# Performance work log

Hardware: AMD Instinct MI355X
Metric: run time of the kernel (lower is better)

## Reference

```python
import jax, jax.numpy as jnp
import numpy as np


def setup_inputs() -> dict:
    key = jax.random.key(0)
    k1, k2 = jax.random.split(key)
    b, c, h, w = 16, 2048, 32, 32
    n_points = 64
    fea = jax.random.normal(k1, (b, c, h, w), dtype=jnp.float32)
    point_list = jax.random.uniform(k2, (n_points, 2), dtype=jnp.float32)  # (x, y) in [0,1)
    valid = jnp.ones((n_points,), dtype=bool)
    return {"fea": fea, "point_list": point_list, "valid": valid}


def reference(fea, point_list, valid):
    # forward_point of SimModel, with fea == backbone(x)['feat4']
    b, c, h, w = fea.shape
    # point_cur = [int(px*w), int(py*h)]  (points in [0,1) so trunc == floor)
    ix = jnp.clip((point_list[:, 0] * w).astype(jnp.int32), 0, w - 1)  # [P]
    iy = jnp.clip((point_list[:, 1] * h).astype(jnp.int32), 0, h - 1)  # [P]
    # gather query feature vectors at each point: [b, c, P]
    queries = fea[:, :, iy, ix]
    # cosine-normalize keys (over channel) and queries
    keys = fea / jnp.linalg.norm(fea, axis=1, keepdims=True)          # [b, c, h, w]
    q = queries / jnp.linalg.norm(queries, axis=1, keepdims=True)    # [b, c, P]
    # cosine-similarity attention over all h*w locations: [b, P, h*w]
    attn = jnp.einsum('bcp,bck->bpk', q, keys.reshape(b, c, h * w))
    # torch: attn = (attn - attn.min(-1)[0]) / attn.max(-1)[0]
    # (RHS fully evaluated first -> both min and max taken on the ORIGINAL attn)
    amin = attn.min(axis=-1, keepdims=True)
    amax = attn.max(axis=-1, keepdims=True)
    attn = (attn - amin) / amax
    soft_masks = attn.reshape(b, -1, h, w)                            # [b, P, h, w]
    # invalid points produce all-zero masks
    return jnp.where(valid[None, :, None, None], soft_masks, jnp.zeros((), soft_masks.dtype))
```

## Files before the change

### kernel.cpp

```cpp
#include <hip/hip_runtime.h>

#define BB 16
#define CC 2048
#define HH 32
#define WW 32
#define HW 1024
#define NP 64

#define PCH 32
#define NCH (CC/PCH)

#define KB 64
#define CT 64
#define BP 68

typedef __bf16 bf16x8  __attribute__((ext_vector_type(8)));
typedef float  f32x4   __attribute__((ext_vector_type(4)));
typedef float  f32x16  __attribute__((ext_vector_type(16)));

__device__ __forceinline__ unsigned f2bf2(float lo, float hi) {
    unsigned a = __float_as_uint(lo);
    unsigned b = __float_as_uint(hi);
    a += 0x7fffu + ((a >> 16) & 1u);
    b += 0x7fffu + ((b >> 16) & 1u);
    return (a >> 16) | (b & 0xffff0000u);
}


__global__ __launch_bounds__(256) void prep_kernel(const float* __restrict__ fea,
                                                   const float* __restrict__ pl,
                                                   unsigned short* __restrict__ qbf,
                                                   float* __restrict__ np2) {
    int cch = blockIdx.x, b = blockIdx.y;
    int t = threadIdx.x, lane = t & 63, rr = t >> 6;

    int ix = (int)(pl[2 * lane + 0] * WW); ix = min(max(ix, 0), WW - 1);
    int iy = (int)(pl[2 * lane + 1] * HH); iy = min(max(iy, 0), HH - 1);
    int kp = iy * WW + ix;

    __shared__ unsigned short buf[2][4][HW];
    __shared__ unsigned short ex[NP][PCH + 4];

    float ssq[16];
#pragma unroll
    for (int i = 0; i < 16; ++i) ssq[i] = 0.f;

    const float* base = fea + ((size_t)b * CC + cch * PCH + rr) * HW + 4 * lane;

#pragma unroll
    for (int ph = 0; ph < PCH / 4; ++ph) {
        float4 fv[4];
#pragma unroll
        for (int s = 0; s < 4; ++s)
            fv[s] = *(const float4*)(base + (size_t)(ph * 4) * HW + 256 * s);
#pragma unroll
        for (int s = 0; s < 4; ++s) {
            ssq[4 * s + 0] += fv[s].x * fv[s].x;
            ssq[4 * s + 1] += fv[s].y * fv[s].y;
            ssq[4 * s + 2] += fv[s].z * fv[s].z;
            ssq[4 * s + 3] += fv[s].w * fv[s].w;
            uint2 pk;
            pk.x = f2bf2(fv[s].x, fv[s].y);
            pk.y = f2bf2(fv[s].z, fv[s].w);
            *(uint2*)&buf[ph & 1][rr][4 * lane + 256 * s] = pk;
        }
        __syncthreads();
        ex[lane][ph * 4 + rr] = buf[ph & 1][rr][kp];
    }
    __syncthreads();

    float* red = (float*)buf;
#pragma unroll
    for (int s = 0; s < 4; ++s) {
        f32x4 v = {ssq[4 * s + 0], ssq[4 * s + 1], ssq[4 * s + 2], ssq[4 * s + 3]};
        *(f32x4*)&red[rr * HW + 4 * lane + 256 * s] = v;
    }
    __syncthreads();
    {
        int k0 = 4 * t;
        f32x4 r0 = *(f32x4*)&red[0 * HW + k0];
        f32x4 r1 = *(f32x4*)&red[1 * HW + k0];
        f32x4 r2 = *(f32x4*)&red[2 * HW + k0];
        f32x4 r3 = *(f32x4*)&red[3 * HW + k0];
        f32x4 sum = (r0 + r1) + (r2 + r3);
        *(f32x4*)&np2[((size_t)cch * BB + b) * HW + k0] = sum;
    }
    {
        int p = t >> 2, part = t & 3;
        uint2 lo = *(uint2*)&ex[p][8 * part];
        uint2 hi = *(uint2*)&ex[p][8 * part + 4];
        uint4 o = make_uint4(lo.x, lo.y, hi.x, hi.y);
        *(uint4*)&qbf[((size_t)b * NP + p) * CC + cch * PCH + 8 * part] = o;
    }
}

__global__ __launch_bounds__(128) void nred_kernel(const float* __restrict__ np2,
                                                   float* __restrict__ rn) {
    int b = blockIdx.y;
    int k = blockIdx.x * 128 + threadIdx.x;
    float s = 0.f;
#pragma unroll 8
    for (int cch = 0; cch < NCH; ++cch)
        s += np2[((size_t)cch * BB + b) * HW + k];
    rn[(size_t)b * HW + k] = rsqrtf(s);
}

template<int NCS>
__global__ __launch_bounds__(256) void gemm_kernel(const float* __restrict__ fea,
                                                   const unsigned short* __restrict__ qbf,
                                                   float* __restrict__ dotp) {
    constexpr int CHALF = CC / NCS;
    constexpr int NST = CHALF / CT;
    constexpr int CSB = (NCS == 4) ? 2 : 1;

    int id = blockIdx.x + (int)gridDim.x * blockIdx.y;
    int cpx = (16 * NCS * BB) >> 3;
    int sid = (id & 7) * cpx + (id >> 3);
    int kc = sid & 15;
    int cs = (sid >> 4) & (NCS - 1);
    int b  = sid >> (4 + CSB);

    int t = threadIdx.x, lane = t & 63, w = t >> 6;
    int pt = w >> 1, kt = w & 1;
    int p0 = 32 * pt;
    int k0 = KB * kc;
    int c0 = cs * CHALF;
    int lo = lane & 31, hi = lane >> 5;

    __shared__ __align__(16) unsigned short bt[2][CT][BP];

    int sc = t >> 2, sq = t & 3;
    const float* gsrc = fea + ((size_t)b * CC + c0 + sc) * HW + k0 + 16 * sq;

    const unsigned short* qb = qbf + ((size_t)b * NP + p0 + lo) * CC + c0 + 8 * hi;

    f32x16 acc = {};
    union UA { int4 i; bf16x8 v; };

    float4 g[4];
#pragma unroll
    for (int h = 0; h < 4; ++h) g[h] = *(const float4*)(gsrc + 4 * h);
    UA a_cur[4], a_nxt[4];
#pragma unroll
    for (int cw = 0; cw < 4; ++cw) a_cur[cw].i = *(const int4*)(qb + 16 * cw);

    for (int s = 0; s < NST; ++s) {
        int cur = s & 1;
#pragma unroll
        for (int h = 0; h < 4; ++h) {
            uint2 pk;
            pk.x = f2bf2(g[h].x, g[h].y);
            pk.y = f2bf2(g[h].z, g[h].w);
            *(uint2*)&bt[cur][sc][16 * sq + 4 * h] = pk;
        }
        __syncthreads();

        int sn = (s + 1 < NST) ? s + 1 : s;
#pragma unroll
        for (int h = 0; h < 4; ++h)
            g[h] = *(const float4*)(gsrc + (size_t)sn * CT * HW + 4 * h);
#pragma unroll
        for (int cw = 0; cw < 4; ++cw)
            a_nxt[cw].i = *(const int4*)(qb + (size_t)sn * CT + 16 * cw);

#pragma unroll
        for (int cw = 0; cw < 4; ++cw) {
            union { unsigned short u[8]; bf16x8 v; } bf;
#pragma unroll
            for (int e = 0; e < 8; ++e)
                bf.u[e] = bt[cur][16 * cw + 8 * hi + e][32 * kt + lo];
            acc = __builtin_amdgcn_mfma_f32_32x32x16_bf16(a_cur[cw].v, bf.v, acc, 0, 0, 0);
        }
#pragma unroll
        for (int cw = 0; cw < 4; ++cw) a_cur[cw] = a_nxt[cw];
    }

    float* dbase = dotp + (((size_t)cs * BB + b) * NP) * HW;
#pragma unroll
    for (int r = 0; r < 16; ++r) {
        int p = p0 + (r & 3) + 8 * (r >> 2) + 4 * hi;
        dbase[(size_t)p * HW + k0 + 32 * kt + lo] = acc[r];
    }
}

template<int NCS>
__global__ __launch_bounds__(256) void finalize_kernel(const float* __restrict__ dotp,
                                                       const float* __restrict__ rn,
                                                       const float* __restrict__ pl,
                                                       const int* __restrict__ valid,
                                                       float* __restrict__ out) {
    int p = blockIdx.x, b = blockIdx.y;
    int t = threadIdx.x;
    int k0 = 4 * t;

    int ix = (int)(pl[2 * p + 0] * WW); ix = min(max(ix, 0), WW - 1);
    int iy = (int)(pl[2 * p + 1] * HH); iy = min(max(iy, 0), HH - 1);
    int kp = iy * WW + ix;
    float rnp = rn[(size_t)b * HW + kp];

    f32x4 d = {0.f, 0.f, 0.f, 0.f};
#pragma unroll
    for (int cs = 0; cs < NCS; ++cs)
        d += *(const f32x4*)(dotp + (((size_t)cs * BB + b) * NP + p) * HW + k0);
    float4 rk = *(const float4*)&rn[(size_t)b * HW + k0];

    float val[4];
    val[0] = d[0] * rk.x * rnp;
    val[1] = d[1] * rk.y * rnp;
    val[2] = d[2] * rk.z * rnp;
    val[3] = d[3] * rk.w * rnp;

    float mn = fminf(fminf(val[0], val[1]), fminf(val[2], val[3]));
    float mx = fmaxf(fmaxf(val[0], val[1]), fmaxf(val[2], val[3]));
#pragma unroll
    for (int off = 32; off; off >>= 1) {
        mn = fminf(mn, __shfl_xor(mn, off));
        mx = fmaxf(mx, __shfl_xor(mx, off));
    }
    __shared__ float smn[4], smx[4];
    int wave = t >> 6;
    if ((t & 63) == 0) { smn[wave] = mn; smx[wave] = mx; }
    __syncthreads();
    mn = fminf(fminf(smn[0], smn[1]), fminf(smn[2], smn[3]));
    mx = fmaxf(fmaxf(smx[0], smx[1]), fmaxf(smx[2], smx[3]));

    bool vld = valid[p] != 0;
    float4 o;
    o.x = vld ? (val[0] - mn) / mx : 0.f;
    o.y = vld ? (val[1] - mn) / mx : 0.f;
    o.z = vld ? (val[2] - mn) / mx : 0.f;
    o.w = vld ? (val[3] - mn) / mx : 0.f;
    *(float4*)&out[((size_t)b * NP + p) * HW + k0] = o;
}

extern "C" void kernel_launch(void* const* d_in, const int* in_sizes, int n_in,
                              void* d_out, int out_size, void* d_ws, size_t ws_size,
                              hipStream_t stream) {
    const float* fea = (const float*)d_in[0];
    const float* pl  = (const float*)d_in[1];
    const int* valid = (const int*)d_in[2];
    float* out = (float*)d_out;

    unsigned short* qbf = (unsigned short*)d_ws;
    float* np2 = (float*)(qbf + (size_t)BB * NP * CC);
    float* rn  = np2 + (size_t)NCH * BB * HW;
    float* dotp = rn + (size_t)BB * HW;

    const size_t base_b = ((size_t)BB * NP * CC) * 2 + ((size_t)NCH * BB * HW + (size_t)BB * HW) * 4;
    const size_t need4 = base_b + (size_t)4 * BB * NP * HW * 4;

    prep_kernel<<<dim3(NCH, BB), 256, 0, stream>>>(fea, pl, qbf, np2);
    nred_kernel<<<dim3(8, BB), 128, 0, stream>>>(np2, rn);
    if (ws_size >= need4) {
        gemm_kernel<4><<<dim3(64, BB), 256, 0, stream>>>(fea, qbf, dotp);
        finalize_kernel<4><<<dim3(NP, BB), 256, 0, stream>>>(dotp, rn, pl, valid, out);
    } else {
        gemm_kernel<2><<<dim3(32, BB), 256, 0, stream>>>(fea, qbf, dotp);
        finalize_kernel<2><<<dim3(NP, BB), 256, 0, stream>>>(dotp, rn, pl, valid, out);
    }
}
```

Measured before the change: 64.23 us.

## Pre-pack features to channel-interleaved bf16 and feed MFMA directly from global

Adds a prep pass that converts the feature map once into a bf16 layout with 8 channels interleaved per spatial location, plus per-chunk squared norms. A separate gather kernel builds the query vectors. The GEMM then loads MFMA B operands straight from this packed buffer, with no LDS staging, barriers or per-tile fp32-to-bf16 conversion. This needs a larger workspace plus an extra 64MB write and read, and it falls back to the old path when the workspace is too small.

```diff
diff --git a/kernel.cpp b/kernel.cpp
--- a/kernel.cpp
+++ b/kernel.cpp
@@ -7,9 +7,7 @@
 #define HW 1024
 #define NP 64
 
-#define PCH 32
-#define NCH (CC/PCH)
-
+#define NCH 64
 #define KB 64
 #define CT 64
 #define BP 68
@@ -27,6 +25,119 @@
 }
 
 
+__global__ __launch_bounds__(256) void prepT_kernel(const float* __restrict__ fea,
+                                                    unsigned short* __restrict__ feaP,
+                                                    float* __restrict__ np2) {
+    int cch = blockIdx.x, b = blockIdx.y;
+    int t = threadIdx.x;
+    int c0 = cch * 32;
+
+    const float* fb = fea + ((size_t)b * CC + c0) * HW + t;
+    unsigned short* fp = feaP + (((size_t)b * 256 + (c0 >> 3)) * HW + t) * 8;
+
+    float ssq[4] = {0.f, 0.f, 0.f, 0.f};
+
+#pragma unroll
+    for (int c8 = 0; c8 < 4; ++c8) {
+#pragma unroll
+        for (int m = 0; m < 4; ++m) {
+            float v[8];
+#pragma unroll
+            for (int e = 0; e < 8; ++e)
+                v[e] = fb[(size_t)(8 * c8 + e) * HW + 256 * m];
+            float s = 0.f;
+#pragma unroll
+            for (int e = 0; e < 8; ++e) s += v[e] * v[e];
+            ssq[m] += s;
+            uint4 o;
+            o.x = f2bf2(v[0], v[1]); o.y = f2bf2(v[2], v[3]);
+            o.z = f2bf2(v[4], v[5]); o.w = f2bf2(v[6], v[7]);
+            *(uint4*)&fp[((size_t)c8 * HW + 256 * m) * 8] = o;
+        }
+    }
+#pragma unroll
+    for (int m = 0; m < 4; ++m)
+        np2[((size_t)cch * BB + b) * HW + t + 256 * m] = ssq[m];
+}
+
+__global__ __launch_bounds__(256) void qgather_kernel(const unsigned short* __restrict__ feaP,
+                                                      const float* __restrict__ pl,
+                                                      unsigned short* __restrict__ qbf) {
+    int p = blockIdx.x, b = blockIdx.y, t = threadIdx.x;
+    int ix = (int)(pl[2 * p + 0] * WW); ix = min(max(ix, 0), WW - 1);
+    int iy = (int)(pl[2 * p + 1] * HH); iy = min(max(iy, 0), HH - 1);
+    int kp = iy * WW + ix;
+    uint4 v = *(const uint4*)&feaP[(((size_t)b * 256 + t) * HW + kp) * 8];
+    *(uint4*)&qbf[((size_t)(b * NP + p)) * CC + 8 * t] = v;
+}
+
+__global__ __launch_bounds__(128) void nred_kernel(const float* __restrict__ np2,
+                                                   float* __restrict__ rn) {
+    int b = blockIdx.y;
+    int k = blockIdx.x * 128 + threadIdx.x;
+    float s = 0.f;
+#pragma unroll 8
+    for (int cch = 0; cch < NCH; ++cch)
+        s += np2[((size_t)cch * BB + b) * HW + k];
+    rn[(size_t)b * HW + k] = rsqrtf(s);
+}
+
+template<int NCS>
+__global__ __launch_bounds__(256) void gemmf_kernel(const unsigned short* __restrict__ feaP,
+                                                    const unsigned short* __restrict__ qbf,
+                                                    float* __restrict__ dotp) {
+    constexpr int CHALF = CC / NCS;
+    constexpr int NST = CHALF / CT;
+    constexpr int CSB = (NCS == 4) ? 2 : 1;
+
+    int id = blockIdx.x + (int)gridDim.x * blockIdx.y;
+    int cpx = (16 * NCS * BB) >> 3;
+    int sid = (id & 7) * cpx + (id >> 3);
+    int kc = sid & 15;
+    int cs = (sid >> 4) & (NCS - 1);
+    int b  = sid >> (4 + CSB);
+
+    int t = threadIdx.x, lane = t & 63, w = t >> 6;
+    int pt = w >> 1, kt = w & 1;
+    int p0 = 32 * pt, k0 = KB * kc, c0 = cs * CHALF;
+    int lo = lane & 31, hi = lane >> 5;
+
+    const unsigned short* qb = qbf + ((size_t)(b * NP + p0 + lo)) * CC + c0 + 8 * hi;
+    const unsigned short* fp = feaP + (((size_t)b * 256 + (c0 >> 3) + hi) * HW
+                                       + k0 + 32 * kt + lo) * 8;
+
+    f32x16 acc = {};
+    union U { int4 i; bf16x8 v; };
+    U a_cur[4], b_cur[4], a_nxt[4], b_nxt[4];
+
+#pragma unroll
+    for (int cw = 0; cw < 4; ++cw) {
+        a_cur[cw].i = *(const int4*)(qb + 16 * cw);
+        b_cur[cw].i = *(const int4*)(fp + (size_t)(2 * cw) * (HW * 8));
+    }
+
+    for (int s = 0; s < NST; ++s) {
+        int sn = (s + 1 < NST) ? s + 1 : s;
+#pragma unroll
+        for (int cw = 0; cw < 4; ++cw) {
+            a_nxt[cw].i = *(const int4*)(qb + sn * CT + 16 * cw);
+            b_nxt[cw].i = *(const int4*)(fp + (size_t)(8 * sn + 2 * cw) * (HW * 8));
+        }
+#pragma unroll
+        for (int cw = 0; cw < 4; ++cw)
+            acc = __builtin_amdgcn_mfma_f32_32x32x16_bf16(a_cur[cw].v, b_cur[cw].v, acc, 0, 0, 0);
+#pragma unroll
+        for (int cw = 0; cw < 4; ++cw) { a_cur[cw] = a_nxt[cw]; b_cur[cw] = b_nxt[cw]; }
+    }
+
+    float* dbase = dotp + (((size_t)cs * BB + b) * NP) * HW;
+#pragma unroll
+    for (int r = 0; r < 16; ++r) {
+        int p = p0 + (r & 3) + 8 * (r >> 2) + 4 * hi;
+        dbase[(size_t)p * HW + k0 + 32 * kt + lo] = acc[r];
+    }
+}
+
 __global__ __launch_bounds__(256) void prep_kernel(const float* __restrict__ fea,
                                                    const float* __restrict__ pl,
                                                    unsigned short* __restrict__ qbf,
@@ -39,16 +150,16 @@
     int kp = iy * WW + ix;
 
     __shared__ unsigned short buf[2][4][HW];
-    __shared__ unsigned short ex[NP][PCH + 4];
+    __shared__ unsigned short ex[NP][32 + 4];
 
     float ssq[16];
 #pragma unroll
     for (int i = 0; i < 16; ++i) ssq[i] = 0.f;
 
-    const float* base = fea + ((size_t)b * CC + cch * PCH + rr) * HW + 4 * lane;
-
-#pragma unroll
-    for (int ph = 0; ph < PCH / 4; ++ph) {
+    const float* base = fea + ((size_t)b * CC + cch * 32 + rr) * HW + 4 * lane;
+
+#pragma unroll
+    for (int ph = 0; ph < 8; ++ph) {
         float4 fv[4];
 #pragma unroll
         for (int s = 0; s < 4; ++s)
@@ -90,49 +201,29 @@
         uint2 lo = *(uint2*)&ex[p][8 * part];
         uint2 hi = *(uint2*)&ex[p][8 * part + 4];
         uint4 o = make_uint4(lo.x, lo.y, hi.x, hi.y);
-        *(uint4*)&qbf[((size_t)b * NP + p) * CC + cch * PCH + 8 * part] = o;
-    }
-}
-
-__global__ __launch_bounds__(128) void nred_kernel(const float* __restrict__ np2,
-                                                   float* __restrict__ rn) {
-    int b = blockIdx.y;
-    int k = blockIdx.x * 128 + threadIdx.x;
-    float s = 0.f;
-#pragma unroll 8
-    for (int cch = 0; cch < NCH; ++cch)
-        s += np2[((size_t)cch * BB + b) * HW + k];
-    rn[(size_t)b * HW + k] = rsqrtf(s);
-}
-
-template<int NCS>
-__global__ __launch_bounds__(256) void gemm_kernel(const float* __restrict__ fea,
-                                                   const unsigned short* __restrict__ qbf,
-                                                   float* __restrict__ dotp) {
-    constexpr int CHALF = CC / NCS;
-    constexpr int NST = CHALF / CT;
-    constexpr int CSB = (NCS == 4) ? 2 : 1;
-
+        *(uint4*)&qbf[((size_t)(b * NP + p)) * CC + cch * 32 + 8 * part] = o;
+    }
+}
+
+__global__ __launch_bounds__(256) void gemm_lds_kernel(const float* __restrict__ fea,
+                                                       const unsigned short* __restrict__ qbf,
+                                                       float* __restrict__ dotp) {
+    constexpr int NCS = 2, CHALF = CC / 2, NST = CHALF / CT;
     int id = blockIdx.x + (int)gridDim.x * blockIdx.y;
     int cpx = (16 * NCS * BB) >> 3;
     int sid = (id & 7) * cpx + (id >> 3);
-    int kc = sid & 15;
-    int cs = (sid >> 4) & (NCS - 1);
-    int b  = sid >> (4 + CSB);
+    int kc = sid & 15, cs = (sid >> 4) & 1, b = sid >> 5;
 
     int t = threadIdx.x, lane = t & 63, w = t >> 6;
     int pt = w >> 1, kt = w & 1;
-    int p0 = 32 * pt;
-    int k0 = KB * kc;
-    int c0 = cs * CHALF;
+    int p0 = 32 * pt, k0 = KB * kc, c0 = cs * CHALF;
     int lo = lane & 31, hi = lane >> 5;
 
     __shared__ __align__(16) unsigned short bt[2][CT][BP];
 
     int sc = t >> 2, sq = t & 3;
     const float* gsrc = fea + ((size_t)b * CC + c0 + sc) * HW + k0 + 16 * sq;
-
-    const unsigned short* qb = qbf + ((size_t)b * NP + p0 + lo) * CC + c0 + 8 * hi;
+    const unsigned short* qb = qbf + ((size_t)(b * NP + p0 + lo)) * CC + c0 + 8 * hi;
 
     f32x16 acc = {};
     union UA { int4 i; bf16x8 v; };
@@ -154,7 +245,6 @@
             *(uint2*)&bt[cur][sc][16 * sq + 4 * h] = pk;
         }
         __syncthreads();
-
         int sn = (s + 1 < NST) ? s + 1 : s;
 #pragma unroll
         for (int h = 0; h < 4; ++h)
@@ -162,7 +252,6 @@
 #pragma unroll
         for (int cw = 0; cw < 4; ++cw)
             a_nxt[cw].i = *(const int4*)(qb + (size_t)sn * CT + 16 * cw);
-
 #pragma unroll
         for (int cw = 0; cw < 4; ++cw) {
             union { unsigned short u[8]; bf16x8 v; } bf;
@@ -230,7 +319,7 @@
     o.y = vld ? (val[1] - mn) / mx : 0.f;
     o.z = vld ? (val[2] - mn) / mx : 0.f;
     o.w = vld ? (val[3] - mn) / mx : 0.f;
-    *(float4*)&out[((size_t)b * NP + p) * HW + k0] = o;
+    *(float4*)&out[((size_t)(b * NP + p)) * HW + k0] = o;
 }
 
 extern "C" void kernel_launch(void* const* d_in, const int* in_sizes, int n_in,
@@ -245,17 +334,23 @@
     float* np2 = (float*)(qbf + (size_t)BB * NP * CC);
     float* rn  = np2 + (size_t)NCH * BB * HW;
     float* dotp = rn + (size_t)BB * HW;
-
-    const size_t base_b = ((size_t)BB * NP * CC) * 2 + ((size_t)NCH * BB * HW + (size_t)BB * HW) * 4;
-    const size_t need4 = base_b + (size_t)4 * BB * NP * HW * 4;
-
-    prep_kernel<<<dim3(NCH, BB), 256, 0, stream>>>(fea, pl, qbf, np2);
-    nred_kernel<<<dim3(8, BB), 128, 0, stream>>>(np2, rn);
-    if (ws_size >= need4) {
-        gemm_kernel<4><<<dim3(64, BB), 256, 0, stream>>>(fea, qbf, dotp);
+    unsigned short* feaP = (unsigned short*)(dotp + (size_t)4 * BB * NP * HW);
+
+    const size_t needP = (size_t)BB * NP * CC * 2
+                       + ((size_t)NCH * BB * HW + (size_t)BB * HW) * 4
+                       + (size_t)4 * BB * NP * HW * 4
+                       + (size_t)BB * (CC / 8) * HW * 8 * 2;
+
+    if (ws_size >= needP) {
+        prepT_kernel<<<dim3(NCH, BB), 256, 0, stream>>>(fea, feaP, np2);
+        qgather_kernel<<<dim3(NP, BB), 256, 0, stream>>>(feaP, pl, qbf);
+        nred_kernel<<<dim3(8, BB), 128, 0, stream>>>(np2, rn);
+        gemmf_kernel<4><<<dim3(64, BB), 256, 0, stream>>>(feaP, qbf, dotp);
         finalize_kernel<4><<<dim3(NP, BB), 256, 0, stream>>>(dotp, rn, pl, valid, out);
     } else {
-        gemm_kernel<2><<<dim3(32, BB), 256, 0, stream>>>(fea, qbf, dotp);
+        prep_kernel<<<dim3(NCH, BB), 256, 0, stream>>>(fea, pl, qbf, np2);
+        nred_kernel<<<dim3(8, BB), 128, 0, stream>>>(np2, rn);
+        gemm_lds_kernel<<<dim3(32, BB), 256, 0, stream>>>(fea, qbf, dotp);
         finalize_kernel<2><<<dim3(NP, BB), 256, 0, stream>>>(dotp, rn, pl, valid, out);
     }
 }
```

Measured after the change: 72.22 us. 1.12x slower.

## Stage bf16 copy of features in prep kernel and feed GEMM from it

Applied to the files above, without the earlier changes.

The prep kernel, which already converts features to bf16 for the query extraction, now also writes a full bf16 copy of the feature map to workspace. A new GEMM kernel loads these bf16 tiles directly into LDS instead of re-reading fp32 features and converting them. The aim is to halve the bytes the GEMM reads and drop its conversion ALU work, at the cost of an extra 64MB write in prep. The channel split is also fixed at 2 instead of 4, which halves the partial-product traffic into the finalize kernel but also halves the GEMM grid size. The fallback path launches the same GEMM twice.

```diff
diff --git a/kernel.cpp b/kernel.cpp
--- a/kernel.cpp
+++ b/kernel.cpp
@@ -9,9 +9,11 @@
 
 #define PCH 32
 #define NCH (CC/PCH)
-
 #define KB 64
 #define CT 64
+#define NCS 2
+#define CHALF (CC/NCS)
+#define NST (CHALF/CT)
 #define BP 68
 
 typedef __bf16 bf16x8  __attribute__((ext_vector_type(8)));
@@ -27,10 +29,12 @@
 }
 
 
+template<bool WRITE_FB16>
 __global__ __launch_bounds__(256) void prep_kernel(const float* __restrict__ fea,
                                                    const float* __restrict__ pl,
                                                    unsigned short* __restrict__ qbf,
-                                                   float* __restrict__ np2) {
+                                                   float* __restrict__ np2,
+                                                   unsigned short* __restrict__ fb16) {
     int cch = blockIdx.x, b = blockIdx.y;
     int t = threadIdx.x, lane = t & 63, rr = t >> 6;
 
@@ -63,6 +67,10 @@
             pk.x = f2bf2(fv[s].x, fv[s].y);
             pk.y = f2bf2(fv[s].z, fv[s].w);
             *(uint2*)&buf[ph & 1][rr][4 * lane + 256 * s] = pk;
+            if (WRITE_FB16) {
+                *(uint2*)&fb16[((size_t)b * CC + cch * PCH + ph * 4 + rr) * HW
+                               + 4 * lane + 256 * s] = pk;
+            }
         }
         __syncthreads();
         ex[lane][ph * 4 + rr] = buf[ph & 1][rr][kp];
@@ -90,7 +98,7 @@
         uint2 lo = *(uint2*)&ex[p][8 * part];
         uint2 hi = *(uint2*)&ex[p][8 * part + 4];
         uint4 o = make_uint4(lo.x, lo.y, hi.x, hi.y);
-        *(uint4*)&qbf[((size_t)b * NP + p) * CC + cch * PCH + 8 * part] = o;
+        *(uint4*)&qbf[((size_t)(b * NP + p)) * CC + cch * PCH + 8 * part] = o;
     }
 }
 
@@ -105,34 +113,86 @@
     rn[(size_t)b * HW + k] = rsqrtf(s);
 }
 
-template<int NCS>
-__global__ __launch_bounds__(256) void gemm_kernel(const float* __restrict__ fea,
-                                                   const unsigned short* __restrict__ qbf,
-                                                   float* __restrict__ dotp) {
-    constexpr int CHALF = CC / NCS;
-    constexpr int NST = CHALF / CT;
-    constexpr int CSB = (NCS == 4) ? 2 : 1;
-
+__global__ __launch_bounds__(256) void gemm_bf_kernel(const unsigned short* __restrict__ fb16,
+                                                      const unsigned short* __restrict__ qbf,
+                                                      float* __restrict__ dotp) {
     int id = blockIdx.x + (int)gridDim.x * blockIdx.y;
     int cpx = (16 * NCS * BB) >> 3;
     int sid = (id & 7) * cpx + (id >> 3);
-    int kc = sid & 15;
-    int cs = (sid >> 4) & (NCS - 1);
-    int b  = sid >> (4 + CSB);
+    int kc = sid & 15, cs = (sid >> 4) & 1, b = sid >> 5;
 
     int t = threadIdx.x, lane = t & 63, w = t >> 6;
     int pt = w >> 1, kt = w & 1;
-    int p0 = 32 * pt;
-    int k0 = KB * kc;
-    int c0 = cs * CHALF;
+    int p0 = 32 * pt, k0 = KB * kc, c0 = cs * CHALF;
+    int lo = lane & 31, hi = lane >> 5;
+
+    __shared__ __align__(16) unsigned short bt[2][CT][BP];
+
+    int sc = t >> 2, kq = t & 3;
+    const unsigned short* gsrc = fb16 + ((size_t)b * CC + c0 + sc) * HW + k0 + 8 * kq;
+
+    const unsigned short* qb = qbf + ((size_t)(b * NP + p0 + lo)) * CC + c0 + 8 * hi;
+
+    f32x16 acc = {};
+    union UA { int4 i; bf16x8 v; };
+
+    uint4 g0 = *(const uint4*)(gsrc);
+    uint4 g1 = *(const uint4*)(gsrc + 32);
+    UA a_cur[4], a_nxt[4];
+#pragma unroll
+    for (int cw = 0; cw < 4; ++cw) a_cur[cw].i = *(const int4*)(qb + 16 * cw);
+
+    for (int s = 0; s < NST; ++s) {
+        int cur = s & 1;
+        *(uint4*)&bt[cur][sc][8 * kq]      = g0;
+        *(uint4*)&bt[cur][sc][32 + 8 * kq] = g1;
+        __syncthreads();
+
+        int sn = (s + 1 < NST) ? s + 1 : s;
+        g0 = *(const uint4*)(gsrc + (size_t)sn * CT * HW);
+        g1 = *(const uint4*)(gsrc + (size_t)sn * CT * HW + 32);
+#pragma unroll
+        for (int cw = 0; cw < 4; ++cw)
+            a_nxt[cw].i = *(const int4*)(qb + (size_t)sn * CT + 16 * cw);
+
+#pragma unroll
+        for (int cw = 0; cw < 4; ++cw) {
+            union { unsigned short u[8]; bf16x8 v; } bf;
+#pragma unroll
+            for (int e = 0; e < 8; ++e)
+                bf.u[e] = bt[cur][16 * cw + 8 * hi + e][32 * kt + lo];
+            acc = __builtin_amdgcn_mfma_f32_32x32x16_bf16(a_cur[cw].v, bf.v, acc, 0, 0, 0);
+        }
+#pragma unroll
+        for (int cw = 0; cw < 4; ++cw) a_cur[cw] = a_nxt[cw];
+    }
+
+    float* dbase = dotp + (((size_t)cs * BB + b) * NP) * HW;
+#pragma unroll
+    for (int r = 0; r < 16; ++r) {
+        int p = p0 + (r & 3) + 8 * (r >> 2) + 4 * hi;
+        dbase[(size_t)p * HW + k0 + 32 * kt + lo] = acc[r];
+    }
+}
+
+__global__ __launch_bounds__(256) void gemm_lds_kernel(const float* __restrict__ fea,
+                                                       const unsigned short* __restrict__ qbf,
+                                                       float* __restrict__ dotp) {
+    int id = blockIdx.x + (int)gridDim.x * blockIdx.y;
+    int cpx = (16 * NCS * BB) >> 3;
+    int sid = (id & 7) * cpx + (id >> 3);
+    int kc = sid & 15, cs = (sid >> 4) & 1, b = sid >> 5;
+
+    int t = threadIdx.x, lane = t & 63, w = t >> 6;
+    int pt = w >> 1, kt = w & 1;
+    int p0 = 32 * pt, k0 = KB * kc, c0 = cs * CHALF;
     int lo = lane & 31, hi = lane >> 5;
 
     __shared__ __align__(16) unsigned short bt[2][CT][BP];
 
     int sc = t >> 2, sq = t & 3;
     const float* gsrc = fea + ((size_t)b * CC + c0 + sc) * HW + k0 + 16 * sq;
-
-    const unsigned short* qb = qbf + ((size_t)b * NP + p0 + lo) * CC + c0 + 8 * hi;
+    const unsigned short* qb = qbf + ((size_t)(b * NP + p0 + lo)) * CC + c0 + 8 * hi;
 
     f32x16 acc = {};
     union UA { int4 i; bf16x8 v; };
@@ -154,7 +214,6 @@
             *(uint2*)&bt[cur][sc][16 * sq + 4 * h] = pk;
         }
         __syncthreads();
-
         int sn = (s + 1 < NST) ? s + 1 : s;
 #pragma unroll
         for (int h = 0; h < 4; ++h)
@@ -162,7 +221,6 @@
 #pragma unroll
         for (int cw = 0; cw < 4; ++cw)
             a_nxt[cw].i = *(const int4*)(qb + (size_t)sn * CT + 16 * cw);
-
 #pragma unroll
         for (int cw = 0; cw < 4; ++cw) {
             union { unsigned short u[8]; bf16x8 v; } bf;
@@ -183,7 +241,6 @@
     }
 }
 
-template<int NCS>
 __global__ __launch_bounds__(256) void finalize_kernel(const float* __restrict__ dotp,
                                                        const float* __restrict__ rn,
                                                        const float* __restrict__ pl,
@@ -230,7 +287,7 @@
     o.y = vld ? (val[1] - mn) / mx : 0.f;
     o.z = vld ? (val[2] - mn) / mx : 0.f;
     o.w = vld ? (val[3] - mn) / mx : 0.f;
-    *(float4*)&out[((size_t)b * NP + p) * HW + k0] = o;
+    *(float4*)&out[((size_t)(b * NP + p)) * HW + k0] = o;
 }
 
 extern "C" void kernel_launch(void* const* d_in, const int* in_sizes, int n_in,
@@ -245,17 +302,23 @@
     float* np2 = (float*)(qbf + (size_t)BB * NP * CC);
     float* rn  = np2 + (size_t)NCH * BB * HW;
     float* dotp = rn + (size_t)BB * HW;
-
-    const size_t base_b = ((size_t)BB * NP * CC) * 2 + ((size_t)NCH * BB * HW + (size_t)BB * HW) * 4;
-    const size_t need4 = base_b + (size_t)4 * BB * NP * HW * 4;
-
-    prep_kernel<<<dim3(NCH, BB), 256, 0, stream>>>(fea, pl, qbf, np2);
-    nred_kernel<<<dim3(8, BB), 128, 0, stream>>>(np2, rn);
-    if (ws_size >= need4) {
-        gemm_kernel<4><<<dim3(64, BB), 256, 0, stream>>>(fea, qbf, dotp);
-        finalize_kernel<4><<<dim3(NP, BB), 256, 0, stream>>>(dotp, rn, pl, valid, out);
+    unsigned short* fb16 = (unsigned short*)(dotp + (size_t)NCS * BB * NP * HW);
+
+    const size_t need = (size_t)BB * NP * CC * 2
+                      + ((size_t)NCH * BB * HW + (size_t)BB * HW) * 4
+                      + (size_t)NCS * BB * NP * HW * 4
+                      + (size_t)BB * CC * HW * 2;
+
+    if (ws_size >= need) {
+        prep_kernel<true><<<dim3(NCH, BB), 256, 0, stream>>>(fea, pl, qbf, np2, fb16);
+        nred_kernel<<<dim3(8, BB), 128, 0, stream>>>(np2, rn);
+        gemm_bf_kernel<<<dim3(16 * NCS, BB), 256, 0, stream>>>(fb16, qbf, dotp);
+        finalize_kernel<<<dim3(NP, BB), 256, 0, stream>>>(dotp, rn, pl, valid, out);
     } else {
-        gemm_kernel<2><<<dim3(32, BB), 256, 0, stream>>>(fea, qbf, dotp);
-        finalize_kernel<2><<<dim3(NP, BB), 256, 0, stream>>>(dotp, rn, pl, valid, out);
-    }
-}
+        prep_kernel<false><<<dim3(NCH, BB), 256, 0, stream>>>(fea, pl, qbf, np2, nullptr);
+        nred_kernel<<<dim3(8, BB), 128, 0, stream>>>(np2, rn);
+        gemm_lds_kernel<<<dim3(16 * NCS, BB), 256, 0, stream>>>(fea, qbf, dotp);
+        gemm_lds_kernel<<<dim3(16 * NCS, BB), 256, 0, stream>>>(fea, qbf, dotp);
+        finalize_kernel<<<dim3(NP, BB), 256, 0, stream>>>(dotp, rn, pl, valid, out);
+    }
+}
```

Measured after the change: 63.31 us. Within noise of the previous version (-1.4%).
